# Kernel optimization log

Hardware: AMD Instinct MI355X
Metric: run time of the kernel (lower is better)

Reference implementation:

```python
import jax, jax.numpy as jnp
import numpy as np

N_NODES = 50000
N_EDGES = 200000
N_GRAPHS = 64
BN_EPS = 1e-5


def _gat(x, src, dst, W, a_src, a_dst, b, heads, ch, concat):
    # x: [N, F_in] -> h: [N, H, C]
    N = x.shape[0]
    h = (x @ W).reshape(N, heads, ch)
    alpha_s = jnp.sum(h * a_src, axis=-1)  # [N, H]
    alpha_d = jnp.sum(h * a_dst, axis=-1)  # [N, H]
    e = jax.nn.leaky_relu(alpha_s[src] + alpha_d[dst], 0.2)  # [E, H]
    # segment softmax over destination nodes
    m = jax.ops.segment_max(e, dst, num_segments=N)  # [N, H]
    e = jnp.exp(e - m[dst])
    s = jax.ops.segment_sum(e, dst, num_segments=N)
    alpha = e / (s[dst] + 1e-16)  # [E, H]
    msg = h[src] * alpha[:, :, None]  # [E, H, C]
    out = jax.ops.segment_sum(msg, dst, num_segments=N)  # [N, H, C]
    out = out.reshape(N, heads * ch) if concat else out.mean(axis=1)
    return out + b


def _bn(x, gamma, beta):
    # eval-mode BatchNorm1d with running_mean=0, running_var=1
    return x * (gamma / jnp.sqrt(1.0 + BN_EPS)) + beta


def _mlp3(g, W1, b1, W2, b2, W3, b3):
    h = jax.nn.relu(g @ W1 + b1)
    h = jax.nn.relu(h @ W2 + b2)
    return h @ W3 + b3


def setup_inputs() -> dict:
    key = jax.random.key(0)
    ks = jax.random.split(key, 48)
    it = iter(range(48))

    def nrm(shape, fan_in):
        return jax.random.normal(ks[next(it)], shape, jnp.float32) / np.sqrt(fan_in)

    x = jax.random.normal(ks[next(it)], (N_NODES, 62), jnp.float32)
    edge_index = jax.random.randint(ks[next(it)], (2, N_EDGES), 0, N_NODES, jnp.int32)
    batch = jnp.sort(jax.random.randint(ks[next(it)], (N_NODES,), 0, N_GRAPHS, jnp.int32))

    d = dict(x=x, edge_index=edge_index, batch=batch)
    d.update(
        Win=nrm((62, 256), 62), b_in=jnp.zeros((256,), jnp.float32),
        W1=nrm((256, 1024), 256), as1=nrm((8, 128), 128), ad1=nrm((8, 128), 128),
        b1=jnp.zeros((1024,), jnp.float32), g1=jnp.ones((1024,), jnp.float32), be1=jnp.zeros((1024,), jnp.float32),
        W2=nrm((1024, 1024), 1024), as2=nrm((8, 128), 128), ad2=nrm((8, 128), 128),
        b2=jnp.zeros((1024,), jnp.float32), g2=jnp.ones((1024,), jnp.float32), be2=jnp.zeros((1024,), jnp.float32),
        W3=nrm((1024, 1024), 1024), as3=nrm((4, 256), 256), ad3=nrm((4, 256), 256),
        b3=jnp.zeros((256,), jnp.float32), g3=jnp.ones((256,), jnp.float32), be3=jnp.zeros((256,), jnp.float32),
        Wp=nrm((768, 256), 768), bp=jnp.zeros((256,), jnp.float32),
        Wv1=nrm((256, 128), 256), bv1=jnp.zeros((128,), jnp.float32),
        Wv2=nrm((128, 64), 128), bv2=jnp.zeros((64,), jnp.float32),
        Wv3=nrm((64, 2), 64), bv3=jnp.zeros((2,), jnp.float32),
        Wt1=nrm((256, 128), 256), bt1=jnp.zeros((128,), jnp.float32),
        Wt2=nrm((128, 64), 128), bt2=jnp.zeros((64,), jnp.float32),
        Wt3=nrm((64, 10), 64), bt3=jnp.zeros((10,), jnp.float32),
        Wc1=nrm((256, 64), 256), bc1=jnp.zeros((64,), jnp.float32),
        Wc2=nrm((64, 1), 64), bc2=jnp.zeros((1,), jnp.float32),
    )
    return d


def reference(x, edge_index, batch, Win, b_in,
              W1, as1, ad1, b1, g1, be1,
              W2, as2, ad2, b2, g2, be2,
              W3, as3, ad3, b3, g3, be3,
              Wp, bp,
              Wv1, bv1, Wv2, bv2, Wv3, bv3,
              Wt1, bt1, Wt2, bt2, Wt3, bt3,
              Wc1, bc1, Wc2, bc2):
    N = x.shape[0]
    loop = jnp.arange(N, dtype=edge_index.dtype)
    src = jnp.concatenate([edge_index[0], loop])  # add_self_loops (PyG default)
    dst = jnp.concatenate([edge_index[1], loop])

    h = jax.nn.relu(x @ Win + b_in)
    x1 = jax.nn.relu(_bn(_gat(h, src, dst, W1, as1, ad1, b1, 8, 128, True), g1, be1))
    x2 = jax.nn.relu(_bn(_gat(x1, src, dst, W2, as2, ad2, b2, 8, 128, True), g2, be2))
    x3 = jax.nn.relu(_bn(_gat(x2, src, dst, W3, as3, ad3, b3, 4, 256, False), g3, be3))

    add_pool = jax.ops.segment_sum(x3, batch, num_segments=N_GRAPHS)
    cnt = jax.ops.segment_sum(jnp.ones((N,), x3.dtype), batch, num_segments=N_GRAPHS)
    mean_pool = add_pool / jnp.maximum(cnt, 1.0)[:, None]
    max_pool = jax.ops.segment_max(x3, batch, num_segments=N_GRAPHS)
    max_pool = jnp.where(jnp.isfinite(max_pool), max_pool, 0.0)

    pooled = jnp.concatenate([mean_pool, max_pool, add_pool], axis=1)  # [G, 768]
    g = jax.nn.relu(pooled @ Wp + bp)

    vuln = _mlp3(g, Wv1, bv1, Wv2, bv2, Wv3, bv3)            # [G, 2]
    vtype = _mlp3(g, Wt1, bt1, Wt2, bt2, Wt3, bt3)           # [G, 10]
    conf = jax.nn.sigmoid(jax.nn.relu(g @ Wc1 + bc1) @ Wc2 + bc2)  # [G, 1]
    return (vuln, vtype, conf)
```

## Files before the change

kernel.cpp:

```cpp
#include <hip/hip_runtime.h>
#include <stdint.h>

static constexpr int NN = 50000;
static constexpr int NP = 50176;
static constexpr int NE = 200000;
static constexpr int NG = 64;
#define BN_S 0.99999500003749968f

typedef __bf16 bf16x8 __attribute__((ext_vector_type(8)));
typedef float  f32x4  __attribute__((ext_vector_type(4)));
typedef __attribute__((address_space(1))) void* as1p;
typedef __attribute__((address_space(3))) void* as3p;
typedef unsigned short u16;

__device__ __forceinline__ float b2f(u16 u){ union{uint32_t i;float f;}x; x.i=((uint32_t)u)<<16; return x.f; }
__device__ __forceinline__ float lo_f(uint32_t u){ union{uint32_t i;float f;}x; x.i=u<<16; return x.f; }
__device__ __forceinline__ float hi_f(uint32_t u){ union{uint32_t i;float f;}x; x.i=u&0xffff0000u; return x.f; }
__device__ __forceinline__ u16 f2b(float f){
  union{float f;uint32_t i;}x; x.f=f;
  return (u16)((x.i + 0x7fffu + ((x.i>>16)&1u)) >> 16);
}
__device__ __forceinline__ void lds_cp16(const void* g, void* l){
  __builtin_amdgcn_global_load_lds((as1p)g, (as3p)l, 16, 0, 0);
}

__global__ void k_detect(const uint32_t* __restrict__ win, int* __restrict__ flag){
  const int lane = threadIdx.x;
  const uint32_t w = win[lane];
  const int e = (w >> 7) & 0xFF;
  const bool band = (e >= 100 && e <= 140) || ((w & 0xFFFFu) == 0u);
  unsigned long long m = __ballot(band);
  if (lane == 0) *flag = (__popcll(m) < 32) ? 1 : 0;
}

struct CvtJobs {
  const void* src[34];
  int n[34];
  int dstoff[34];
  int cum[35];
  int njobs;
  int total;
};
__global__ __launch_bounds__(256) void k_cvt(CvtJobs jobs, const int* __restrict__ flag,
                                             u16* __restrict__ dst0){
  const int i = blockIdx.x*256 + threadIdx.x;
  if (i >= jobs.total) return;
  int lo = 0, hi = jobs.njobs - 1;
  while (lo < hi){ int mid = (lo+hi+1)>>1; if (jobs.cum[mid] <= i) lo = mid; else hi = mid-1; }
  const int j = lo;
  const int e = i - jobs.cum[j];
  u16 v = (*flag) ? f2b(((const float*)jobs.src[j])[e]) : ((const u16*)jobs.src[j])[e];
  dst0[jobs.dstoff[j] + e] = v;
}

__global__ void k_pad_x(const void* __restrict__ x, u16* __restrict__ xp, const int* __restrict__ flag){
  int i = blockIdx.x*256 + threadIdx.x;
  if (i >= NP*64) return;
  int n = i >> 6, k = i & 63;
  u16 v = 0;
  if (n < NN && k < 62)
    v = (*flag) ? f2b(((const float*)x)[n*62 + k]) : ((const u16*)x)[n*62 + k];
  xp[i] = v;
}
__global__ void k_pad_winT(const void* __restrict__ w, u16* __restrict__ wt, const int* __restrict__ flag){
  int i = blockIdx.x*256 + threadIdx.x;
  if (i >= 256*64) return;
  int o = i >> 6, k = i & 63;
  u16 v = 0;
  if (k < 62)
    v = (*flag) ? f2b(((const float*)w)[k*256 + o]) : ((const u16*)w)[k*256 + o];
  wt[i] = v;
}
__global__ __launch_bounds__(256) void k_transpose_t(const void* __restrict__ w, u16* __restrict__ wt,
                                                     int K, int NO, const int* __restrict__ flag){
  __shared__ u16 t[64][65];
  const int k0 = blockIdx.x * 64;
  const int o0 = blockIdx.y * 64;
  const int tx = threadIdx.x & 63;
  const int ty = threadIdx.x >> 6;
  const bool f32 = (*flag) != 0;
  #pragma unroll
  for (int kk = ty; kk < 64; kk += 4){
    const int k = k0 + kk, o = o0 + tx;
    u16 v = 0;
    if (k < K && o < NO)
      v = f32 ? f2b(((const float*)w)[(size_t)k*NO + o]) : ((const u16*)w)[(size_t)k*NO + o];
    t[kk][tx] = v;
  }
  __syncthreads();
  #pragma unroll
  for (int oo = ty; oo < 64; oo += 4){
    const int o = o0 + oo, k = k0 + tx;
    if (o < NO && k < K)
      wt[(size_t)o*K + k] = t[tx][oo];
  }
}

__global__ void k_init_counts(int* counts){
  int i = blockIdx.x*256 + threadIdx.x;
  if (i < NN) counts[i] = 1;
}
__global__ void k_count(const int* __restrict__ eidx, int* counts){
  int e = blockIdx.x*256 + threadIdx.x;
  if (e < NE) atomicAdd(&counts[eidx[NE + e]], 1);
}
__global__ __launch_bounds__(1024) void k_scan(const int* __restrict__ counts,
                                               int* __restrict__ indptr, int* __restrict__ cursor){
  __shared__ int sums[1024];
  const int t = threadIdx.x;
  const int strip = (NN + 1023)/1024;
  int lo = t*strip, hi = lo+strip < NN ? lo+strip : NN;
  int s = 0;
  for (int i=lo;i<hi;i++) s += counts[i];
  sums[t] = s; __syncthreads();
  for (int off=1; off<1024; off<<=1){
    int v = (t>=off) ? sums[t-off] : 0;
    __syncthreads();
    sums[t] += v;
    __syncthreads();
  }
  int base = t ? sums[t-1] : 0;
  for (int i=lo;i<hi;i++){ indptr[i]=base; cursor[i]=base; base += counts[i]; }
  if (t == 1023) indptr[NN] = sums[1023];
}
__global__ void k_fill(const int* __restrict__ eidx, int* cursor, int* __restrict__ srcs){
  int i = blockIdx.x*256 + threadIdx.x;
  if (i >= NE + NN) return;
  int s, d;
  if (i < NE){ s = eidx[i]; d = eidx[NE+i]; }
  else { s = d = i - NE; }
  int p = atomicAdd(&cursor[d], 1);
  srcs[p] = s;
}

template<int K, bool EPI, int BNSH>
__global__ __launch_bounds__(256) void k_gemm_bt(const u16* __restrict__ A, const u16* __restrict__ B,
                                                 u16* __restrict__ C, int ldc, const u16* __restrict__ bias){
  __shared__ __align__(16) u16 As[128*64];
  __shared__ __align__(16) u16 Bs[128*64];
  const int tid = threadIdx.x;
  const int lane = tid & 63, wv = tid >> 6;
  const int bid = blockIdx.x;
  const size_t bm = bid >> BNSH, bn = bid & ((1<<BNSH)-1);
  const u16* Ab = A + bm*128*(size_t)K;
  const u16* Bb = B + bn*128*(size_t)K;
  f32x4 acc[4][4] = {};
  const int wm = (wv>>1)*64, wn = (wv&1)*64;
  const int r = lane & 15, kg = lane >> 4;
  const int srow = wv*32 + (lane>>3);
  const int scol = (lane&7)*8;
  for (int kt = 0; kt < K; kt += 64){
    #pragma unroll
    for (int i=0;i<4;i++){
      lds_cp16(Ab + (size_t)(srow + i*8)*K + kt + scol, (char*)As + (wv*4+i)*1024);
      lds_cp16(Bb + (size_t)(srow + i*8)*K + kt + scol, (char*)Bs + (wv*4+i)*1024);
    }
    __syncthreads();
    #pragma unroll
    for (int ks=0; ks<2; ks++){
      bf16x8 a[4], b[4];
      const int ko = ks*32 + kg*8;
      #pragma unroll
      for (int i=0;i<4;i++) a[i] = *(const bf16x8*)(As + (wm + i*16 + r)*64 + ko);
      #pragma unroll
      for (int j=0;j<4;j++) b[j] = *(const bf16x8*)(Bs + (wn + j*16 + r)*64 + ko);
      #pragma unroll
      for (int i=0;i<4;i++)
        #pragma unroll
        for (int j=0;j<4;j++)
          acc[i][j] = __builtin_amdgcn_mfma_f32_16x16x32_bf16(a[i], b[j], acc[i][j], 0, 0, 0);
    }
    __syncthreads();
  }
  const int rg = lane>>4, cl = lane&15;
  #pragma unroll
  for (int i=0;i<4;i++){
    #pragma unroll
    for (int j=0;j<4;j++){
      const int col = (int)bn*128 + wn + j*16 + cl;
      float bv = 0.f;
      if (EPI) bv = b2f(bias[col]);
      #pragma unroll
      for (int rr=0;rr<4;rr++){
        const int row = (int)bm*128 + wm + i*16 + rg*4 + rr;
        float v = acc[i][j][rr];
        if (EPI){ v += bv; v = v>0.f ? v : 0.f; }
        C[(size_t)row*ldc + col] = f2b(v);
      }
    }
  }
}

template<int K, int BNT>
__global__ __launch_bounds__(512, 2) void k_gemm256(const u16* __restrict__ A, const u16* __restrict__ B,
                                                    u16* __restrict__ C, int ldc){
  __shared__ __align__(16) u16 lds[65536];
  const int tid = threadIdx.x;
  const int lane = tid & 63, wid = tid >> 6;
  const int wr = wid >> 2, wc = wid & 3;
  const int cpx = gridDim.x >> 3;
  const int b = (blockIdx.x & 7)*cpx + (blockIdx.x >> 3);
  const int bm = b / BNT, bn = b % BNT;
  const u16* Ab = A + (size_t)bm*256*K;
  const u16* Bb = B + (size_t)bn*256*K;
  const int r = lane & 15, kg = lane >> 4;
  const int r7 = r & 7;
  f32x4 acc[8][4] = {};

  auto stage = [&](int which, int T, int wro){
    const u16* src = (which < 2 ? Ab + (size_t)(which*128)*K
                                : Bb + (size_t)((which-2)*128)*K) + (size_t)T*64;
    u16* dst = lds + wro + (which >= 2 ? 16384 : 0) + (which & 1)*8192;
    const int gslot = (tid & 7) ^ ((tid >> 3) & 7);
    #pragma unroll
    for (int L = 0; L < 2; L++){
      const int off = L*4096 + tid*8;
      lds_cp16(src + (size_t)(off >> 6)*K + gslot*8, dst + off);
    }
  };

  auto do_tile = [&](int T, int rdo, int wro, bool prefetch){
    const u16* As_ = lds + rdo;
    const u16* Bs_ = lds + rdo + 16384;
    #pragma unroll
    for (int ks = 0; ks < 2; ++ks){
      const int sl = ((ks*4 + kg) ^ r7) * 8;
      bf16x8 b2[4];
      const u16* bp = Bs_ + (wc*64 + r)*64 + sl;
      #pragma unroll
      for (int n = 0; n < 4; n++) b2[n] = *(const bf16x8*)(bp + n*1024);
      #pragma unroll
      for (int h = 0; h < 2; ++h){
        const int p = ks*2 + h;
        bf16x8 a[4];
        const u16* ap = As_ + (wr*128 + h*64 + r)*64 + sl;
        #pragma unroll
        for (int m = 0; m < 4; m++) a[m] = *(const bf16x8*)(ap + m*1024);
        if (prefetch){
          if (p == 0){ stage(0, T+1, wro); stage(1, T+1, wro); }
          else if (p == 1){ stage(2, T+1, wro); stage(3, T+1, wro); }
        }
        __builtin_amdgcn_s_barrier();
        __builtin_amdgcn_s_setprio(1);
        #pragma unroll
        for (int m = 0; m < 4; m++)
          #pragma unroll
          for (int n = 0; n < 4; n++)
            acc[h*4+m][n] = __builtin_amdgcn_mfma_f32_16x16x32_bf16(a[m], b2[n], acc[h*4+m][n], 0, 0, 0);
        __builtin_amdgcn_s_setprio(0);
        if (p < 3) __builtin_amdgcn_s_barrier();
        else       __syncthreads();
      }
    }
  };

  constexpr int NT = K/64;
  stage(0,0,0); stage(1,0,0); stage(2,0,0); stage(3,0,0);
  __syncthreads();
  for (int T = 0; T < NT; T += 2){
    do_tile(T,     0,     32768, true);
    do_tile(T+1, 32768,   0,     T+2 < NT);
  }

  const int cl = lane & 15, rg = lane >> 4;
  #pragma unroll
  for (int h = 0; h < 2; h++)
    #pragma unroll
    for (int m = 0; m < 4; m++)
      #pragma unroll
      for (int n = 0; n < 4; n++){
        const int col = bn*256 + wc*64 + n*16 + cl;
        #pragma unroll
        for (int rr = 0; rr < 4; rr++){
          const int row = bm*256 + wr*128 + h*64 + m*16 + rg*4 + rr;
          C[(size_t)row*ldc + col] = f2b(acc[h*4+m][n][rr]);
        }
      }
}

template<int H>
__global__ __launch_bounds__(256) void k_alpha(const u16* __restrict__ h,
                                               const u16* __restrict__ a_s, const u16* __restrict__ a_d,
                                               float* __restrict__ os, float* __restrict__ od){
  const int n = blockIdx.x*4 + (threadIdx.x>>6);
  if (n >= NN) return;
  const int lane = threadIdx.x & 63;
  const int c0 = lane*16;
  const uint4 hv0 = *(const uint4*)(h + (size_t)n*1024 + c0);
  const uint4 hv1 = *(const uint4*)(h + (size_t)n*1024 + c0 + 8);
  const uint4 sv0 = *(const uint4*)(a_s + c0);
  const uint4 sv1 = *(const uint4*)(a_s + c0 + 8);
  const uint4 dv0 = *(const uint4*)(a_d + c0);
  const uint4 dv1 = *(const uint4*)(a_d + c0 + 8);
  float ss = 0.f, sd = 0.f;
  uint32_t hu[8] = {hv0.x,hv0.y,hv0.z,hv0.w,hv1.x,hv1.y,hv1.z,hv1.w};
  uint32_t su[8] = {sv0.x,sv0.y,sv0.z,sv0.w,sv1.x,sv1.y,sv1.z,sv1.w};
  uint32_t du[8] = {dv0.x,dv0.y,dv0.z,dv0.w,dv1.x,dv1.y,dv1.z,dv1.w};
  #pragma unroll
  for (int q=0;q<8;q++){
    float h0 = lo_f(hu[q]), h1 = hi_f(hu[q]);
    ss += h0*lo_f(su[q]) + h1*hi_f(su[q]);
    sd += h0*lo_f(du[q]) + h1*hi_f(du[q]);
  }
  const int G = 64 / H;
  #pragma unroll
  for (int off=1; off<G; off<<=1){ ss += __shfl_xor(ss, off); sd += __shfl_xor(sd, off); }
  if ((lane & (G-1)) == 0){
    os[n*H + lane/G] = ss;
    od[n*H + lane/G] = sd;
  }
}

template<int H>
__global__ __launch_bounds__(256) void k_soft(const float* __restrict__ asb, const float* __restrict__ adb,
                                              const int* __restrict__ indptr, const int* __restrict__ srcs,
                                              float* __restrict__ wbuf, float* __restrict__ invs){
  const int idx = blockIdx.x*256 + threadIdx.x;
  if (idx >= NN*H) return;
  const int n = idx / H, hh = idx - n*H;
  const float adn = adb[idx];
  const int p0 = indptr[n], p1 = indptr[n+1];
  float m = -1e30f;
  for (int p = p0; p < p1; ++p){
    float t = asb[srcs[p]*H + hh] + adn;
    float v = t > 0.f ? t : 0.2f*t;
    m = fmaxf(m, v);
  }
  float s = 0.f;
  for (int p = p0; p < p1; ++p){
    float t = asb[srcs[p]*H + hh] + adn;
    float v = t > 0.f ? t : 0.2f*t;
    float e = __expf(v - m);
    wbuf[(size_t)p*H + hh] = e;
    s += e;
  }
  invs[idx] = 1.0f/(s + 1e-16f);
}

template<int H, int C, bool FINAL>
__global__ __launch_bounds__(256) void k_agg2(const u16* __restrict__ h,
                                              const float* __restrict__ wbuf, const float* __restrict__ invs,
                                              const int* __restrict__ indptr, const int* __restrict__ srcs,
                                              const u16* __restrict__ bias, const u16* __restrict__ gamma,
                                              const u16* __restrict__ beta, u16* __restrict__ out){
  const int n = blockIdx.x;
  const int tid = threadIdx.x;
  constexpr int OUTW = FINAL ? C : H*C;
  if (n >= NN){
    for (int c = tid; c < OUTW; c += 256) out[(size_t)n*OUTW + c] = 0;
    return;
  }
  const int p0 = indptr[n], p1 = indptr[n+1];
  if (!FINAL){
    const int c0 = tid*4;
    const int hd = c0 >> 7;
    float a0=0.f,a1=0.f,a2=0.f,a3=0.f;
    int p = p0;
    for (; p + 2 <= p1; p += 2){
      const int s0 = srcs[p], s1 = srcs[p+1];
      const float w0 = wbuf[(size_t)p*H + hd];
      const float w1 = wbuf[(size_t)(p+1)*H + hd];
      const ushort4 v0 = *(const ushort4*)(h + (size_t)s0*1024 + c0);
      const ushort4 v1 = *(const ushort4*)(h + (size_t)s1*1024 + c0);
      a0 += w0*b2f(v0.x) + w1*b2f(v1.x);
      a1 += w0*b2f(v0.y) + w1*b2f(v1.y);
      a2 += w0*b2f(v0.z) + w1*b2f(v1.z);
      a3 += w0*b2f(v0.w) + w1*b2f(v1.w);
    }
    if (p < p1){
      const int s0 = srcs[p];
      const float w0 = wbuf[(size_t)p*H + hd];
      const ushort4 v0 = *(const ushort4*)(h + (size_t)s0*1024 + c0);
      a0 += w0*b2f(v0.x); a1 += w0*b2f(v0.y); a2 += w0*b2f(v0.z); a3 += w0*b2f(v0.w);
    }
    const float is = invs[n*H + hd];
    float vv[4] = {a0,a1,a2,a3};
    u16 ov[4];
    #pragma unroll
    for (int i2=0;i2<4;i2++){
      const int c = c0 + i2;
      float v = (vv[i2]*is + b2f(bias[c])) * (b2f(gamma[c])*BN_S) + b2f(beta[c]);
      ov[i2] = f2b(v>0.f ? v : 0.f);
    }
    *(ushort4*)(out + (size_t)n*1024 + c0) = make_ushort4(ov[0],ov[1],ov[2],ov[3]);
  } else {
    const int c = tid;
    float a0=0.f,a1=0.f,a2=0.f,a3=0.f;
    for (int p = p0; p < p1; ++p){
      const int s = srcs[p];
      const float4 w4 = *(const float4*)(wbuf + (size_t)p*4);
      const u16* hr = h + (size_t)s*1024 + c;
      a0 += w4.x * b2f(hr[0]);
      a1 += w4.y * b2f(hr[256]);
      a2 += w4.z * b2f(hr[512]);
      a3 += w4.w * b2f(hr[768]);
    }
    const float4 is = *(const float4*)(invs + n*4);
    float meanv = 0.25f*(a0*is.x + a1*is.y + a2*is.z + a3*is.w);
    float v = (meanv + b2f(bias[c])) * (b2f(gamma[c])*BN_S) + b2f(beta[c]);
    out[(size_t)n*C + c] = f2b(v>0.f ? v : 0.f);
  }
}

__global__ __launch_bounds__(256) void k_pool_init(float* __restrict__ pooled, int* __restrict__ gcnt){
  int i = blockIdx.x*256 + threadIdx.x;
  if (i < NG*768) pooled[i] = 0.f;
  if (i < NG) gcnt[i] = 0;
}
__global__ __launch_bounds__(256) void k_pool1(const u16* __restrict__ x3, const int* __restrict__ batch,
                                               float* __restrict__ pooled, int* __restrict__ gcnt){
  const int n0 = blockIdx.x*64;
  const int n1 = (n0+64 < NN) ? n0+64 : NN;
  if (n0 >= NN) return;
  const int t = threadIdx.x;
  float sum=0.f, mx=0.f;
  int curg = batch[n0];
  int segstart = n0;
  for (int n=n0; n<n1; ++n){
    const int g = batch[n];
    if (g != curg){
      atomicAdd(&pooled[curg*768+512+t], sum);
      atomicMax((unsigned int*)&pooled[curg*768+256+t], __float_as_uint(mx));
      if (t==0) atomicAdd(&gcnt[curg], n-segstart);
      sum=0.f; mx=0.f; curg=g; segstart=n;
    }
    float v = b2f(x3[(size_t)n*256+t]);
    sum += v; mx = fmaxf(mx, v);
  }
  atomicAdd(&pooled[curg*768+512+t], sum);
  atomicMax((unsigned int*)&pooled[curg*768+256+t], __float_as_uint(mx));
  if (t==0) atomicAdd(&gcnt[curg], n1-segstart);
}
__global__ __launch_bounds__(256) void k_pool_fin(float* __restrict__ pooled, const int* __restrict__ gcnt){
  int i = blockIdx.x*256 + threadIdx.x;
  if (i >= NG*256) return;
  int g = i>>8, c = i&255;
  float s = pooled[g*768+512+c];
  int cnt = gcnt[g];
  pooled[g*768+c] = s / (float)(cnt>1?cnt:1);
}

__global__ __launch_bounds__(256) void k_gvec(const float* __restrict__ pooled, const u16* __restrict__ Wp,
                                              const u16* __restrict__ bp, float* __restrict__ gbuf){
  const int g = blockIdx.x, t = threadIdx.x;
  __shared__ float ps[768];
  for (int i=t;i<768;i+=256) ps[i] = pooled[g*768+i];
  __syncthreads();
  float acc = b2f(bp[t]);
  for (int k=0;k<768;k++) acc += ps[k]*b2f(Wp[k*256+t]);
  gbuf[g*256+t] = acc>0.f ? acc : 0.f;
}
__global__ __launch_bounds__(128) void k_heads(const float* __restrict__ gbuf,
    const u16* Wv1,const u16* bv1,const u16* Wv2,const u16* bv2,const u16* Wv3,const u16* bv3,
    const u16* Wt1,const u16* bt1,const u16* Wt2,const u16* bt2,const u16* Wt3,const u16* bt3,
    const u16* Wc1,const u16* bc1,const u16* Wc2,const u16* bc2,
    void* __restrict__ outp, const int* __restrict__ flag){
  const int g = blockIdx.x, t = threadIdx.x;
  const int f32o = *flag;
  u16* o16 = (u16*)outp;
  float* o32 = (float*)outp;
  __shared__ float gs[256], h1[128], h2[64];
  gs[t] = gbuf[g*256+t]; gs[t+128] = gbuf[g*256+t+128];
  __syncthreads();
  { float a = b2f(bv1[t]); for (int k=0;k<256;k++) a += gs[k]*b2f(Wv1[k*128+t]); h1[t] = a>0.f?a:0.f; }
  __syncthreads();
  if (t<64){ float a=b2f(bv2[t]); for(int k=0;k<128;k++) a += h1[k]*b2f(Wv2[k*64+t]); h2[t]=a>0.f?a:0.f; }
  __syncthreads();
  if (t<2){ float a=b2f(bv3[t]); for(int k=0;k<64;k++) a += h2[k]*b2f(Wv3[k*2+t]);
            if (f32o) o32[g*2+t]=a; else o16[g*2+t]=f2b(a); }
  __syncthreads();
  { float a = b2f(bt1[t]); for (int k=0;k<256;k++) a += gs[k]*b2f(Wt1[k*128+t]); h1[t] = a>0.f?a:0.f; }
  __syncthreads();
  if (t<64){ float a=b2f(bt2[t]); for(int k=0;k<128;k++) a += h1[k]*b2f(Wt2[k*64+t]); h2[t]=a>0.f?a:0.f; }
  __syncthreads();
  if (t<10){ float a=b2f(bt3[t]); for(int k=0;k<64;k++) a += h2[k]*b2f(Wt3[k*10+t]);
             if (f32o) o32[128 + g*10+t]=a; else o16[128 + g*10+t]=f2b(a); }
  __syncthreads();
  if (t<64){ float a=b2f(bc1[t]); for(int k=0;k<256;k++) a += gs[k]*b2f(Wc1[k*64+t]); h2[t]=a>0.f?a:0.f; }
  __syncthreads();
  if (t==0){
    float a=b2f(bc2[0]);
    for(int k=0;k<64;k++) a += h2[k]*b2f(Wc2[k]);
    float r = 1.f/(1.f+__expf(-a));
    if (f32o) o32[768+g]=r; else o16[768+g]=f2b(r);
  }
}

extern "C" void kernel_launch(void* const* d_in, const int* in_sizes, int n_in,
                              void* d_out, int out_size, void* d_ws, size_t ws_size,
                              hipStream_t stream){
  (void)in_sizes; (void)n_in; (void)out_size; (void)ws_size;
  const int* eidx = (const int*)d_in[1];
  const int* batch= (const int*)d_in[2];

  char* ws = (char*)d_ws;
  size_t off = 0;
  auto alloc = [&](size_t bytes) -> void* {
    void* p = ws + off;
    off += (bytes + 255) & ~(size_t)255;
    return p;
  };
  u16* bufA  = (u16*)alloc((size_t)NP*1024*2);
  u16* bufH  = (u16*)alloc((size_t)NP*1024*2);
  u16* W1t   = (u16*)alloc((size_t)1024*256*2);
  u16* W2t   = (u16*)alloc((size_t)1024*1024*2);
  u16* W3t   = (u16*)alloc((size_t)1024*1024*2);
  u16* WinT  = (u16*)alloc((size_t)256*64*2);
  const size_t wbytes = ((size_t)(NE+NN)*8*4 + 255) & ~(size_t)255;
  const size_t ibytes = (size_t)NN*8*4;
  const size_t xbytes = (size_t)NP*64*2;
  char* un = (char*)alloc(wbytes + ibytes > xbytes ? wbytes + ibytes : xbytes);
  u16*   Xp   = (u16*)un;
  float* wbuf = (float*)un;
  float* invs = (float*)(un + wbytes);
  float* asb = (float*)alloc((size_t)NN*8*4);
  float* adb = (float*)alloc((size_t)NN*8*4);
  int* counts= (int*)alloc((size_t)NN*4);
  int* cursor= (int*)alloc((size_t)NN*4);
  int* indptr= (int*)alloc((size_t)(NN+1)*4);
  int* srcs  = (int*)alloc((size_t)(NE+NN)*4);
  float* pooled = (float*)alloc((size_t)NG*768*4);
  float* gbuf   = (float*)alloc((size_t)NG*256*4);
  int* gcnt  = (int*)alloc((size_t)NG*4);
  u16* cvt   = (u16*)alloc((size_t)320*1024*2);
  int* flag  = (int*)alloc(256);

  CvtJobs jobs; int ji = 0; int cvtoff = 0; int cume = 0;
  auto addjob = [&](int idx, int n) -> u16* {
    jobs.src[ji] = d_in[idx]; jobs.n[ji] = n; jobs.dstoff[ji] = cvtoff;
    jobs.cum[ji] = cume; cume += n; ji++;
    u16* r = cvt + cvtoff; cvtoff = (cvtoff + n + 15) & ~15; return r;
  };
  u16* cb_in= addjob(4, 256);
  u16* cas1 = addjob(6, 1024);  u16* cad1 = addjob(7, 1024);
  u16* cb1  = addjob(8, 1024);  u16* cg1  = addjob(9, 1024);  u16* cbe1 = addjob(10, 1024);
  u16* cas2 = addjob(12, 1024); u16* cad2 = addjob(13, 1024);
  u16* cb2  = addjob(14, 1024); u16* cg2  = addjob(15, 1024); u16* cbe2 = addjob(16, 1024);
  u16* cas3 = addjob(18, 1024); u16* cad3 = addjob(19, 1024);
  u16* cb3  = addjob(20, 256);  u16* cg3  = addjob(21, 256);  u16* cbe3 = addjob(22, 256);
  u16* cWp  = addjob(23, 196608); u16* cbp = addjob(24, 256);
  u16* cWv1 = addjob(25, 32768);  u16* cbv1= addjob(26, 128);
  u16* cWv2 = addjob(27, 8192);   u16* cbv2= addjob(28, 64);
  u16* cWv3 = addjob(29, 128);    u16* cbv3= addjob(30, 2);
  u16* cWt1 = addjob(31, 32768);  u16* cbt1= addjob(32, 128);
  u16* cWt2 = addjob(33, 8192);   u16* cbt2= addjob(34, 64);
  u16* cWt3 = addjob(35, 640);    u16* cbt3= addjob(36, 10);
  u16* cWc1 = addjob(37, 16384);  u16* cbc1= addjob(38, 64);
  u16* cWc2 = addjob(39, 64);     u16* cbc2= addjob(40, 1);
  jobs.cum[ji] = cume; jobs.njobs = ji; jobs.total = cume;

  k_detect<<<1, 64, 0, stream>>>((const uint32_t*)d_in[3], flag);
  k_cvt<<<(cume+255)/256, 256, 0, stream>>>(jobs, flag, cvt);
  k_pad_x<<<(NP*64+255)/256, 256, 0, stream>>>(d_in[0], Xp, flag);
  k_pad_winT<<<(256*64+255)/256, 256, 0, stream>>>(d_in[3], WinT, flag);
  k_transpose_t<<<dim3(4,16), 256, 0, stream>>>(d_in[5], W1t, 256, 1024, flag);
  k_transpose_t<<<dim3(16,16), 256, 0, stream>>>(d_in[11], W2t, 1024, 1024, flag);
  k_transpose_t<<<dim3(16,16), 256, 0, stream>>>(d_in[17], W3t, 1024, 1024, flag);

  k_init_counts<<<(NN+255)/256, 256, 0, stream>>>(counts);
  k_count<<<(NE+255)/256, 256, 0, stream>>>(eidx, counts);
  k_scan<<<1, 1024, 0, stream>>>(counts, indptr, cursor);
  k_fill<<<(NE+NN+255)/256, 256, 0, stream>>>(eidx, cursor, srcs);

  k_gemm_bt<64,true,1><<<dim3((NP/128)*2), 256, 0, stream>>>(Xp, WinT, bufA, 256, cb_in);

  k_gemm256<256,4><<<dim3((NP/256)*4), 512, 0, stream>>>(bufA, W1t, bufH, 1024);
  k_alpha<8><<<(NN+3)/4, 256, 0, stream>>>(bufH, cas1, cad1, asb, adb);
  k_soft<8><<<(NN*8+255)/256, 256, 0, stream>>>(asb, adb, indptr, srcs, wbuf, invs);
  k_agg2<8,128,false><<<NP, 256, 0, stream>>>(bufH, wbuf, invs, indptr, srcs, cb1, cg1, cbe1, bufA);

  k_gemm256<1024,4><<<dim3((NP/256)*4), 512, 0, stream>>>(bufA, W2t, bufH, 1024);
  k_alpha<8><<<(NN+3)/4, 256, 0, stream>>>(bufH, cas2, cad2, asb, adb);
  k_soft<8><<<(NN*8+255)/256, 256, 0, stream>>>(asb, adb, indptr, srcs, wbuf, invs);
  k_agg2<8,128,false><<<NP, 256, 0, stream>>>(bufH, wbuf, invs, indptr, srcs, cb2, cg2, cbe2, bufA);

  k_gemm256<1024,4><<<dim3((NP/256)*4), 512, 0, stream>>>(bufA, W3t, bufH, 1024);
  k_alpha<4><<<(NN+3)/4, 256, 0, stream>>>(bufH, cas3, cad3, asb, adb);
  k_soft<4><<<(NN*4+255)/256, 256, 0, stream>>>(asb, adb, indptr, srcs, wbuf, invs);
  k_agg2<4,256,true><<<NP, 256, 0, stream>>>(bufH, wbuf, invs, indptr, srcs, cb3, cg3, cbe3, bufA);

  k_pool_init<<<(NG*768+255)/256, 256, 0, stream>>>(pooled, gcnt);
  k_pool1<<<(NN+63)/64, 256, 0, stream>>>(bufA, batch, pooled, gcnt);
  k_pool_fin<<<(NG*256+255)/256, 256, 0, stream>>>(pooled, gcnt);
  k_gvec<<<NG, 256, 0, stream>>>(pooled, cWp, cbp, gbuf);
  k_heads<<<NG, 128, 0, stream>>>(gbuf, cWv1,cbv1,cWv2,cbv2,cWv3,cbv3,
                                  cWt1,cbt1,cWt2,cbt2,cWt3,cbt3, cWc1,cbc1,cWc2,cbc2,
                                  d_out, flag);
}
```

Before: 935.4 us.

## Restructure GEMM main loop into 4-slot, K=32 ring buffer with vmcnt waits

The 256x256 bf16 GEMM drops its double-buffered K=64 tiles with several barriers per tile. It now uses a 4-slot LDS ring of K=32 tiles, keeping three loads in flight and waiting on vmcnt counts, so each step needs only one barrier. The XOR swizzle is reworked for the 32-wide rows. This aims to overlap global-to-LDS loads with MFMA and cut barrier stalls, at the cost of a finer K step that does fewer MFMAs per barrier.

New measurement: 916.4 us. -2.0%, faster.

```diff
diff --git a/kernel.cpp b/kernel.cpp
--- a/kernel.cpp
+++ b/kernel.cpp
@@ -204,78 +204,65 @@
   const u16* Ab = A + (size_t)bm*256*K;
   const u16* Bb = B + (size_t)bn*256*K;
   const int r = lane & 15, kg = lane >> 4;
-  const int r7 = r & 7;
+  const int rs = (r >> 1) & 3;
   f32x4 acc[8][4] = {};
 
-  auto stage = [&](int which, int T, int wro){
-    const u16* src = (which < 2 ? Ab + (size_t)(which*128)*K
-                                : Bb + (size_t)((which-2)*128)*K) + (size_t)T*64;
-    u16* dst = lds + wro + (which >= 2 ? 16384 : 0) + (which & 1)*8192;
-    const int gslot = (tid & 7) ^ ((tid >> 3) & 7);
-    #pragma unroll
-    for (int L = 0; L < 2; L++){
-      const int off = L*4096 + tid*8;
-      lds_cp16(src + (size_t)(off >> 6)*K + gslot*8, dst + off);
-    }
+  const int gslot = (tid & 3) ^ ((tid >> 3) & 3);
+  const int srow0 = tid >> 2;
+  const int srow1 = 128 + (tid >> 2);
+  auto stage = [&](int T, int slot){
+    u16* dstA = lds + slot*16384 + tid*8;
+    u16* dstB = dstA + 8192;
+    const size_t kof = (size_t)T*32 + gslot*8;
+    lds_cp16(Ab + (size_t)srow0*K + kof, dstA);
+    lds_cp16(Ab + (size_t)srow1*K + kof, dstA + 4096);
+    lds_cp16(Bb + (size_t)srow0*K + kof, dstB);
+    lds_cp16(Bb + (size_t)srow1*K + kof, dstB + 4096);
   };
 
-  auto do_tile = [&](int T, int rdo, int wro, bool prefetch){
-    const u16* As_ = lds + rdo;
-    const u16* Bs_ = lds + rdo + 16384;
-    #pragma unroll
-    for (int ks = 0; ks < 2; ++ks){
-      const int sl = ((ks*4 + kg) ^ r7) * 8;
-      bf16x8 b2[4];
-      const u16* bp = Bs_ + (wc*64 + r)*64 + sl;
+  auto do_tile = [&](int slot){
+    const u16* As_ = lds + slot*16384;
+    const u16* Bs_ = As_ + 8192;
+    const int sl = (kg ^ rs) * 8;
+    bf16x8 bfr[4];
+    const u16* bp = Bs_ + (wc*64 + r)*32 + sl;
+    #pragma unroll
+    for (int n = 0; n < 4; n++) bfr[n] = *(const bf16x8*)(bp + n*512);
+    __builtin_amdgcn_s_setprio(1);
+    #pragma unroll
+    for (int m = 0; m < 8; m++){
+      bf16x8 a = *(const bf16x8*)(As_ + (wr*128 + m*16 + r)*32 + sl);
       #pragma unroll
-      for (int n = 0; n < 4; n++) b2[n] = *(const bf16x8*)(bp + n*1024);
-      #pragma unroll
-      for (int h = 0; h < 2; ++h){
-        const int p = ks*2 + h;
-        bf16x8 a[4];
-        const u16* ap = As_ + (wr*128 + h*64 + r)*64 + sl;
-        #pragma unroll
-        for (int m = 0; m < 4; m++) a[m] = *(const bf16x8*)(ap + m*1024);
-        if (prefetch){
-          if (p == 0){ stage(0, T+1, wro); stage(1, T+1, wro); }
-          else if (p == 1){ stage(2, T+1, wro); stage(3, T+1, wro); }
-        }
-        __builtin_amdgcn_s_barrier();
-        __builtin_amdgcn_s_setprio(1);
-        #pragma unroll
-        for (int m = 0; m < 4; m++)
-          #pragma unroll
-          for (int n = 0; n < 4; n++)
-            acc[h*4+m][n] = __builtin_amdgcn_mfma_f32_16x16x32_bf16(a[m], b2[n], acc[h*4+m][n], 0, 0, 0);
-        __builtin_amdgcn_s_setprio(0);
-        if (p < 3) __builtin_amdgcn_s_barrier();
-        else       __syncthreads();
-      }
-    }
+      for (int n = 0; n < 4; n++)
+        acc[m][n] = __builtin_amdgcn_mfma_f32_16x16x32_bf16(a, bfr[n], acc[m][n], 0, 0, 0);
+    }
+    __builtin_amdgcn_s_setprio(0);
   };
 
-  constexpr int NT = K/64;
-  stage(0,0,0); stage(1,0,0); stage(2,0,0); stage(3,0,0);
-  __syncthreads();
-  for (int T = 0; T < NT; T += 2){
-    do_tile(T,     0,     32768, true);
-    do_tile(T+1, 32768,   0,     T+2 < NT);
+  constexpr int NT = K/32;
+  stage(0,0); stage(1,1); stage(2,2);
+  for (int T = 0; T < NT; ++T){
+    if (T + 2 < NT)      asm volatile("s_waitcnt vmcnt(8)" ::: "memory");
+    else if (T + 1 < NT) asm volatile("s_waitcnt vmcnt(4)" ::: "memory");
+    else                 asm volatile("s_waitcnt vmcnt(0)" ::: "memory");
+    __builtin_amdgcn_s_barrier();
+    __builtin_amdgcn_sched_barrier(0);
+    if (T + 3 < NT) stage(T+3, (T+3)&3);
+    do_tile(T & 3);
   }
 
   const int cl = lane & 15, rg = lane >> 4;
   #pragma unroll
-  for (int h = 0; h < 2; h++)
-    #pragma unroll
-    for (int m = 0; m < 4; m++)
+  for (int m = 0; m < 8; m++)
+    #pragma unroll
+    for (int n = 0; n < 4; n++){
+      const int col = bn*256 + wc*64 + n*16 + cl;
       #pragma unroll
-      for (int n = 0; n < 4; n++){
-        const int col = bn*256 + wc*64 + n*16 + cl;
-        #pragma unroll
-        for (int rr = 0; rr < 4; rr++){
-          const int row = bm*256 + wr*128 + h*64 + m*16 + rg*4 + rr;
-          C[(size_t)row*ldc + col] = f2b(acc[h*4+m][n][rr]);
-        }
+      for (int rr = 0; rr < 4; rr++){
+        const int row = bm*256 + wr*128 + m*16 + rg*4 + rr;
+        C[(size_t)row*ldc + col] = f2b(acc[m][n][rr]);
       }
+    }
 }
 
 template<int H>
```
